# Performance work log

Measured on AMD Instinct MI355X. Metric: run time of the kernel, lower is better.

## Reference

```python
import jax, jax.numpy as jnp
import numpy as np

B, H, W = 4, 256, 256
DIM, DIM_OUT, NUM_HEADS = 96, 192, 3
WS = 8            # window_size
QS = 2            # q_stride (2,2)
HIDDEN = int(DIM_OUT * 4.0)
EPS = 1e-6


def layernorm(x, g, b):
    m = jnp.mean(x, axis=-1, keepdims=True)
    v = jnp.mean(jnp.square(x - m), axis=-1, keepdims=True)
    return (x - m) * jax.lax.rsqrt(v + EPS) * g + b


def maxpool2x2(x):
    # x: [..., h, w, c] -> [..., h//2, w//2, c]
    s = x.shape
    x = x.reshape(s[:-3] + (s[-3] // QS, QS, s[-2] // QS, QS, s[-1]))
    return x.max(axis=(-4, -2))


def setup_inputs() -> dict:
    key = jax.random.key(0)
    ks = jax.random.split(key, 16)
    std = 0.02
    return {
        "x": jax.random.normal(ks[0], (B, H, W, DIM), dtype=jnp.float32),
        "norm1_g": jnp.ones((DIM,), jnp.float32),
        "norm1_b": jnp.zeros((DIM,), jnp.float32),
        "proj_w": jax.random.normal(ks[1], (DIM, DIM_OUT), jnp.float32) * std,
        "proj_b": jnp.zeros((DIM_OUT,), jnp.float32),
        "qkv_w": jax.random.normal(ks[2], (DIM, 3 * DIM_OUT), jnp.float32) * std,
        "qkv_b": jnp.zeros((3 * DIM_OUT,), jnp.float32),
        "attn_proj_w": jax.random.normal(ks[3], (DIM_OUT, DIM_OUT), jnp.float32) * std,
        "attn_proj_b": jnp.zeros((DIM_OUT,), jnp.float32),
        "norm2_g": jnp.ones((DIM_OUT,), jnp.float32),
        "norm2_b": jnp.zeros((DIM_OUT,), jnp.float32),
        "mlp_w1": jax.random.normal(ks[4], (DIM_OUT, HIDDEN), jnp.float32) * std,
        "mlp_b1": jnp.zeros((HIDDEN,), jnp.float32),
        "mlp_w2": jax.random.normal(ks[5], (HIDDEN, DIM_OUT), jnp.float32) * std,
        "mlp_b2": jnpp_zeros if False else jnp.zeros((DIM_OUT,), jnp.float32),
    }


def reference(x, norm1_g, norm1_b, proj_w, proj_b, qkv_w, qkv_b,
              attn_proj_w, attn_proj_b, norm2_g, norm2_b,
              mlp_w1, mlp_b1, mlp_w2, mlp_b2):
    b, h, w, _ = x.shape
    xn = layernorm(x, norm1_g, norm1_b)

    # dim != dim_out: shortcut = proj(norm(x)), then pooled by q_stride
    shortcut = xn @ proj_w + proj_b                       # [B,H,W,Do]
    shortcut = maxpool2x2(shortcut)                       # [B,H/2,W/2,Do]

    # window partition (H,W divisible by WS -> no padding)
    nh, nw = h // WS, w // WS
    xw = xn.reshape(b, nh, WS, nw, WS, DIM).transpose(0, 1, 3, 2, 4, 5)
    xw = xw.reshape(b * nh * nw, WS, WS, DIM)             # [Bw,WS,WS,C]
    Bw = xw.shape[0]

    # MultiScaleAttention with q pooling
    hd = DIM_OUT // NUM_HEADS
    qkv = (xw @ qkv_w + qkv_b).reshape(Bw, WS * WS, 3, NUM_HEADS, hd)
    q, k, v = qkv[:, :, 0], qkv[:, :, 1], qkv[:, :, 2]    # [Bw,N,h,d]
    q = maxpool2x2(q.reshape(Bw, WS, WS, DIM_OUT))        # [Bw,WS/2,WS/2,Do]
    wq = WS // QS
    q = q.reshape(Bw, wq * wq, NUM_HEADS, hd)

    scale = 1.0 / jnp.sqrt(jnp.asarray(hd, x.dtype))
    scores = jnp.einsum('bqhd,bkhd->bhqk', q, k) * scale
    probs = jax.nn.softmax(scores, axis=-1)
    out = jnp.einsum('bhqk,bkhd->bqhd', probs, v).reshape(Bw, wq, wq, DIM_OUT)
    out = out @ attn_proj_w + attn_proj_b                 # [Bw,wq,wq,Do]

    # window unpartition at pooled resolution
    hp, wp = h // QS, w // QS
    out = out.reshape(b, nh, nw, wq, wq, DIM_OUT).transpose(0, 1, 3, 2, 4, 5)
    out = out.reshape(b, hp, wp, DIM_OUT)

    y = shortcut + out
    yn = layernorm(y, norm2_g, norm2_b)
    mlp = jax.nn.gelu(yn @ mlp_w1 + mlp_b1, approximate=False) @ mlp_w2 + mlp_b2
    return y + mlp
```

## Files before the change

kernel.cpp:

```cpp
#include <hip/hip_runtime.h>
#include <hip/hip_bf16.h>
#include <math.h>

#define EPSV 1e-6f

typedef __attribute__((ext_vector_type(8))) short bf16x8;
typedef __attribute__((ext_vector_type(4))) float f32x4;
typedef __attribute__((ext_vector_type(4))) unsigned short u16x4;
typedef __attribute__((ext_vector_type(2))) unsigned int u32x2;

__device__ inline float bf2f(unsigned short u) {
  union { unsigned int i; float f; } v;
  v.i = ((unsigned int)u) << 16;
  return v.f;
}
__device__ inline unsigned short f2bf(float f) {
  unsigned int u = __builtin_bit_cast(unsigned int, f);
  u += 0x7FFFu + ((u >> 16) & 1u);
  return (unsigned short)(u >> 16);
}
__device__ inline unsigned int pk2(float lo, float hi) {
  unsigned int r;
  asm("v_cvt_pk_bf16_f32 %0, %1, %2" : "=v"(r) : "v"(lo), "v"(hi));
  return r;
}
__device__ inline float fast_gelu(float v) {
  float u = 1.5957691216057308f * (v + 0.044715f * v * v * v);
  float t = __expf(-u);
  return v * __builtin_amdgcn_rcpf(1.f + t);
}

__global__ __launch_bounds__(256) void k0_pack(
    const float* __restrict__ qw, const float* __restrict__ aw,
    const float* __restrict__ w1, const float* __restrict__ w2,
    const float* __restrict__ pw, unsigned short* __restrict__ qwp,
    unsigned short* __restrict__ awp, unsigned short* __restrict__ w1p,
    unsigned short* __restrict__ w2p, unsigned short* __restrict__ pwp) {
  int idx = blockIdx.x * 256 + threadIdx.x;
  int lane = idx & 63;
  int l15 = lane & 15, quad = lane >> 4;
  if (idx < 6912) {
    int fi = idx >> 6;
    int ntile = fi / 3, kstep = fi - ntile * 3;
    int n = ntile * 16 + l15, k0 = kstep * 32 + quad * 8;
#pragma unroll
    for (int j = 0; j < 8; ++j)
      qwp[(size_t)idx * 8 + j] = f2bf(qw[(size_t)(k0 + j) * 576 + n]);
  } else if (idx < 11520) {
    int i2 = idx - 6912;
    int fi = i2 >> 6;
    int ntile = fi / 6, kstep = fi - ntile * 6;
    int n = ntile * 16 + l15, k0 = kstep * 32 + quad * 8;
#pragma unroll
    for (int j = 0; j < 8; ++j)
      awp[(size_t)i2 * 8 + j] = f2bf(aw[(size_t)(k0 + j) * 192 + n]);
  } else if (idx < 29952) {
    int i3 = idx - 11520;
    int fi = i3 >> 6;
    int ntile = fi / 6, kstep = fi - ntile * 6;
    int n = ntile * 16 + l15, k0 = kstep * 32 + quad * 8;
#pragma unroll
    for (int j = 0; j < 8; ++j)
      w1p[(size_t)i3 * 8 + j] = f2bf(w1[(size_t)(k0 + j) * 768 + n]);
  } else if (idx < 48384) {
    int i4 = idx - 29952;
    int fi = i4 >> 6;
    int ntile = fi / 24, kstep = fi - ntile * 24;
    int n = ntile * 16 + l15, k0 = kstep * 32 + quad * 8;
#pragma unroll
    for (int j = 0; j < 8; ++j)
      w2p[(size_t)i4 * 8 + j] = f2bf(w2[(size_t)(k0 + j) * 192 + n]);
  } else if (idx < 50688) {
    int i5 = idx - 48384;
    int fi = i5 >> 6;
    int ntile = fi / 3, kstep = fi - ntile * 3;
    int n = ntile * 16 + l15, k0 = kstep * 32 + quad * 8;
#pragma unroll
    for (int j = 0; j < 8; ++j)
      pwp[(size_t)i5 * 8 + j] = f2bf(pw[(size_t)(k0 + j) * 192 + n]);
  }
}

__global__ __launch_bounds__(256, 4) void k1234_fused(
    const float* __restrict__ x, const float* __restrict__ n1g,
    const float* __restrict__ n1b, const unsigned short* __restrict__ pwp,
    const float* __restrict__ pb, const unsigned short* __restrict__ qwp,
    const float* __restrict__ qb, const unsigned short* __restrict__ awp,
    const float* __restrict__ ab, const float* __restrict__ n2g,
    const float* __restrict__ n2b, const unsigned short* __restrict__ w1p,
    const float* __restrict__ b1, const unsigned short* __restrict__ w2p,
    const float* __restrict__ b2, float* __restrict__ out) {
  __shared__ __align__(16) unsigned char smem[39936];
  unsigned short (*kk)[200] = (unsigned short (*)[200])smem;
  unsigned short (*vT)[72] = (unsigned short (*)[72])smem;
  unsigned short (*yn)[200] = (unsigned short (*)[200])(smem + 6400);
  unsigned short (*hls)[200] = (unsigned short (*)[200])(smem + 12800);
  unsigned short (*wbuf)[16][72] =
      (unsigned short (*)[16][72])(smem + 27648);
  float (*sc)[192] = (float (*)[192])(smem + 27648);

  int tid = threadIdx.x, wave = tid >> 6, lane = tid & 63;
  int wi = blockIdx.x;
  int b = wi >> 10, nh = (wi >> 5) & 31, nw = wi & 31;
  int grow0 = nh * 8, gcol0 = nw * 8;
  int l15 = lane & 15, quad = lane >> 4;

  {
    int tt = tid >> 2, sub = tid & 3;
    int rr = tt >> 3, cc = tt & 7;
    size_t tok = (size_t)((b * 256 + grow0 + rr) * 256 + gcol0 + cc);
    const f32x4* xr4 = (const f32x4*)(x + tok * 96 + sub * 24);
    f32x4 v[6];
#pragma unroll
    for (int i = 0; i < 6; ++i) v[i] = xr4[i];
    float s = 0.f;
#pragma unroll
    for (int i = 0; i < 6; ++i)
#pragma unroll
      for (int j = 0; j < 4; ++j) s += v[i][j];
    s += __shfl_xor(s, 1);
    s += __shfl_xor(s, 2);
    float mean = s * (1.f / 96.f);
    float q = 0.f;
#pragma unroll
    for (int i = 0; i < 6; ++i)
#pragma unroll
      for (int j = 0; j < 4; ++j) {
        float d = v[i][j] - mean;
        q += d * d;
      }
    q += __shfl_xor(q, 1);
    q += __shfl_xor(q, 2);
    float rstd = rsqrtf(q * (1.f / 96.f) + EPSV);
    const f32x4* g4 = (const f32x4*)(n1g + sub * 24);
    const f32x4* b4 = (const f32x4*)(n1b + sub * 24);
#pragma unroll
    for (int i = 0; i < 6; ++i) {
      f32x4 gg = g4[i], bb = b4[i];
      u32x2 w;
      w[0] = pk2((v[i][0] - mean) * rstd * gg[0] + bb[0],
                 (v[i][1] - mean) * rstd * gg[1] + bb[1]);
      w[1] = pk2((v[i][2] - mean) * rstd * gg[2] + bb[2],
                 (v[i][3] - mean) * rstd * gg[3] + bb[3]);
      *(u32x2*)(&kk[tt][sub * 24 + i * 4]) = w;
    }
  }
  __syncthreads();

  bf16x8 areg[4][3];
#pragma unroll
  for (int mt = 0; mt < 4; ++mt)
#pragma unroll
    for (int ks = 0; ks < 3; ++ks)
      areg[mt][ks] = *(const bf16x8*)(&kk[mt * 16 + l15][ks * 32 + quad * 8]);
  __syncthreads();

#pragma unroll
  for (int aj = 0; aj < 6; ++aj) {
    int type, hh, nt;
    if (wave < 3) {
      if (aj < 4) { type = 0; hh = wave; nt = aj; }
      else { int kidx = wave * 2 + (aj - 4); type = 1; hh = kidx >> 2; nt = kidx & 3; }
    } else {
      int kidx = 6 + aj; type = 1; hh = kidx >> 2; nt = kidx & 3;
    }
    int gnt = type * 12 + hh * 4 + nt;
    const unsigned short* bp = qwp + (size_t)gnt * 1536 + lane * 8;
    bf16x8 b0 = *(const bf16x8*)(bp);
    bf16x8 b1v = *(const bf16x8*)(bp + 512);
    bf16x8 b2v = *(const bf16x8*)(bp + 1024);
    int dloc = nt * 16 + l15;
    int dglob = hh * 64 + dloc;
    float bias = qb[type * 192 + dglob];
#pragma unroll
    for (int mt = 0; mt < 4; ++mt) {
      f32x4 acc = {0.f, 0.f, 0.f, 0.f};
      acc = __builtin_amdgcn_mfma_f32_16x16x32_bf16(areg[mt][0], b0, acc, 0, 0, 0);
      acc = __builtin_amdgcn_mfma_f32_16x16x32_bf16(areg[mt][1], b1v, acc, 0, 0, 0);
      acc = __builtin_amdgcn_mfma_f32_16x16x32_bf16(areg[mt][2], b2v, acc, 0, 0, 0);
      if (type == 0) {
        float p0 = fmaxf(acc[0], acc[1]);
        float p1 = fmaxf(acc[2], acc[3]);
        float q0 = fmaxf(p0, __shfl_xor(p0, 32));
        float q1 = fmaxf(p1, __shfl_xor(p1, 32));
        unsigned int uq = pk2(q0 + bias, q1 + bias);
        if (quad < 2) {
          int p = mt * 4 + quad * 2;
          wbuf[wave][p][dloc] = (unsigned short)uq;
          wbuf[wave][p + 1][dloc] = (unsigned short)(uq >> 16);
        }
      } else {
        int t0 = mt * 16 + quad * 4;
        unsigned int u01 = pk2(acc[0] + bias, acc[1] + bias);
        unsigned int u23 = pk2(acc[2] + bias, acc[3] + bias);
        kk[t0 + 0][dglob] = (unsigned short)u01;
        kk[t0 + 1][dglob] = (unsigned short)(u01 >> 16);
        kk[t0 + 2][dglob] = (unsigned short)u23;
        kk[t0 + 3][dglob] = (unsigned short)(u23 >> 16);
      }
    }
  }
  __syncthreads();

  if (wave < 3) {
    int h = wave;
    bf16x8 aq0 = *(const bf16x8*)(&wbuf[wave][l15][quad * 8]);
    bf16x8 aq1 = *(const bf16x8*)(&wbuf[wave][l15][32 + quad * 8]);
    f32x4 s4[4];
#pragma unroll
    for (int kt = 0; kt < 4; ++kt) {
      bf16x8 bk0 = *(const bf16x8*)(&kk[kt * 16 + l15][h * 64 + quad * 8]);
      bf16x8 bk1 = *(const bf16x8*)(&kk[kt * 16 + l15][h * 64 + 32 + quad * 8]);
      f32x4 s = {0.f, 0.f, 0.f, 0.f};
      s = __builtin_amdgcn_mfma_f32_16x16x32_bf16(aq0, bk0, s, 0, 0, 0);
      s = __builtin_amdgcn_mfma_f32_16x16x32_bf16(aq1, bk1, s, 0, 0, 0);
      s4[kt] = s;
    }
    float ps[4][4];
#pragma unroll
    for (int r = 0; r < 4; ++r) {
      float m = fmaxf(fmaxf(s4[0][r], s4[1][r]), fmaxf(s4[2][r], s4[3][r]));
#pragma unroll
      for (int o = 8; o; o >>= 1) m = fmaxf(m, __shfl_xor(m, o));
      float sm = 0.f;
#pragma unroll
      for (int kt = 0; kt < 4; ++kt) {
        float e = __expf((s4[kt][r] - m) * 0.125f);
        ps[kt][r] = e;
        sm += e;
      }
#pragma unroll
      for (int o = 8; o; o >>= 1) sm += __shfl_xor(sm, o);
      float inv = __builtin_amdgcn_rcpf(sm);
#pragma unroll
      for (int kt = 0; kt < 4; ++kt) ps[kt][r] *= inv;
    }
#pragma unroll
    for (int r = 0; r < 4; ++r) {
      int row = quad * 4 + r;
      unsigned int u0 = pk2(ps[0][r], ps[1][r]);
      unsigned int u1 = pk2(ps[2][r], ps[3][r]);
      wbuf[wave][row][l15] = (unsigned short)u0;
      wbuf[wave][row][16 + l15] = (unsigned short)(u0 >> 16);
      wbuf[wave][row][32 + l15] = (unsigned short)u1;
      wbuf[wave][row][48 + l15] = (unsigned short)(u1 >> 16);
    }
  }
  __syncthreads();

#pragma unroll
  for (int vj = 0; vj < 3; ++vj) {
    int vidx = wave * 3 + vj;
    int hh = vidx >> 2, nt = vidx & 3;
    const unsigned short* bp =
        qwp + (size_t)(24 + hh * 4 + nt) * 1536 + lane * 8;
    bf16x8 b0 = *(const bf16x8*)(bp);
    bf16x8 b1v = *(const bf16x8*)(bp + 512);
    bf16x8 b2v = *(const bf16x8*)(bp + 1024);
    int dglob = hh * 64 + nt * 16 + l15;
    float bias = qb[384 + dglob];
#pragma unroll
    for (int mt = 0; mt < 4; ++mt) {
      f32x4 acc = {0.f, 0.f, 0.f, 0.f};
      acc = __builtin_amdgcn_mfma_f32_16x16x32_bf16(areg[mt][0], b0, acc, 0, 0, 0);
      acc = __builtin_amdgcn_mfma_f32_16x16x32_bf16(areg[mt][1], b1v, acc, 0, 0, 0);
      acc = __builtin_amdgcn_mfma_f32_16x16x32_bf16(areg[mt][2], b2v, acc, 0, 0, 0);
      int t0 = mt * 16 + quad * 4;
      u32x2 pk;
      pk[0] = pk2(acc[0] + bias, acc[1] + bias);
      pk[1] = pk2(acc[2] + bias, acc[3] + bias);
      *(u32x2*)(&vT[dglob][t0]) = pk;
    }
  }
  __syncthreads();

  f32x4 o4[4];
  if (wave < 3) {
    int h = wave;
    bf16x8 ap0 = *(const bf16x8*)(&wbuf[wave][l15][quad * 8]);
    bf16x8 ap1 = *(const bf16x8*)(&wbuf[wave][l15][32 + quad * 8]);
#pragma unroll
    for (int dt = 0; dt < 4; ++dt) {
      bf16x8 bv0 = *(const bf16x8*)(&vT[h * 64 + dt * 16 + l15][quad * 8]);
      bf16x8 bv1 = *(const bf16x8*)(&vT[h * 64 + dt * 16 + l15][32 + quad * 8]);
      f32x4 o = {0.f, 0.f, 0.f, 0.f};
      o = __builtin_amdgcn_mfma_f32_16x16x32_bf16(ap0, bv0, o, 0, 0, 0);
      o = __builtin_amdgcn_mfma_f32_16x16x32_bf16(ap1, bv1, o, 0, 0, 0);
      o4[dt] = o;
    }
  }
  __syncthreads();

  if (wave < 3) {
    int h = wave;
#pragma unroll
    for (int r = 0; r < 4; ++r) {
      int row = quad * 4 + r;
      unsigned int u0 = pk2(o4[0][r], o4[1][r]);
      unsigned int u1 = pk2(o4[2][r], o4[3][r]);
      kk[row][h * 64 + l15] = (unsigned short)u0;
      kk[row][h * 64 + 16 + l15] = (unsigned short)(u0 >> 16);
      kk[row][h * 64 + 32 + l15] = (unsigned short)u1;
      kk[row][h * 64 + 48 + l15] = (unsigned short)(u1 >> 16);
    }
  }
#pragma unroll
  for (int nl = 0; nl < 3; ++nl) {
    int nt = wave * 3 + nl;
    const unsigned short* bp = pwp + ((size_t)(nt * 3) * 64 + lane) * 8;
    bf16x8 b0 = *(const bf16x8*)(bp);
    bf16x8 b1v = *(const bf16x8*)(bp + 512);
    bf16x8 b2v = *(const bf16x8*)(bp + 1024);
    int c = nt * 16 + l15;
    float bias = pb[c];
#pragma unroll
    for (int mt = 0; mt < 4; ++mt) {
      f32x4 acc = {0.f, 0.f, 0.f, 0.f};
      acc = __builtin_amdgcn_mfma_f32_16x16x32_bf16(areg[mt][0], b0, acc, 0, 0, 0);
      acc = __builtin_amdgcn_mfma_f32_16x16x32_bf16(areg[mt][1], b1v, acc, 0, 0, 0);
      acc = __builtin_amdgcn_mfma_f32_16x16x32_bf16(areg[mt][2], b2v, acc, 0, 0, 0);
      float p0 = fmaxf(acc[0], acc[1]);
      float p1 = fmaxf(acc[2], acc[3]);
      float q0 = fmaxf(p0, __shfl_xor(p0, 32)) + bias;
      float q1 = fmaxf(p1, __shfl_xor(p1, 32)) + bias;
      if (quad < 2) {
        int p = mt * 4 + quad * 2;
        sc[p][c] = q0;
        sc[p + 1][c] = q1;
      }
    }
  }
  __syncthreads();

  bf16x8 ao[6];
#pragma unroll
  for (int ks = 0; ks < 6; ++ks)
    ao[ks] = *(const bf16x8*)(&kk[l15][ks * 32 + quad * 8]);
#pragma unroll
  for (int nl = 0; nl < 3; ++nl) {
    int ntl = wave * 3 + nl;
    const unsigned short* bp = awp + (size_t)ntl * 3072 + lane * 8;
    f32x4 acc = {0.f, 0.f, 0.f, 0.f};
#pragma unroll
    for (int ks = 0; ks < 6; ++ks) {
      bf16x8 bw = *(const bf16x8*)(bp + ks * 512);
      acc = __builtin_amdgcn_mfma_f32_16x16x32_bf16(ao[ks], bw, acc, 0, 0, 0);
    }
    int cc = ntl * 16 + l15;
    float bias = ab[cc];
#pragma unroll
    for (int r = 0; r < 4; ++r) {
      int p = quad * 4 + r;
      sc[p][cc] += acc[r] + bias;
    }
  }
  __syncthreads();

  {
    int tt = wave * 4 + quad;
    const f32x4* y4 = (const f32x4*)(&sc[tt][l15 * 12]);
    f32x4 vv[3];
    vv[0] = y4[0]; vv[1] = y4[1]; vv[2] = y4[2];
    float s = 0.f;
#pragma unroll
    for (int i = 0; i < 3; ++i)
#pragma unroll
      for (int j = 0; j < 4; ++j) s += vv[i][j];
    s += __shfl_xor(s, 1);
    s += __shfl_xor(s, 2);
    s += __shfl_xor(s, 4);
    s += __shfl_xor(s, 8);
    float mean = s * (1.f / 192.f);
    float q = 0.f;
#pragma unroll
    for (int i = 0; i < 3; ++i)
#pragma unroll
      for (int j = 0; j < 4; ++j) {
        float d = vv[i][j] - mean;
        q += d * d;
      }
    q += __shfl_xor(q, 1);
    q += __shfl_xor(q, 2);
    q += __shfl_xor(q, 4);
    q += __shfl_xor(q, 8);
    float rstd = rsqrtf(q * (1.f / 192.f) + EPSV);
    const f32x4* g4 = (const f32x4*)(n2g + l15 * 12);
    const f32x4* b4 = (const f32x4*)(n2b + l15 * 12);
#pragma unroll
    for (int i = 0; i < 3; ++i) {
      f32x4 gg = g4[i], bb = b4[i];
      u32x2 w;
      w[0] = pk2((vv[i][0] - mean) * rstd * gg[0] + bb[0],
                 (vv[i][1] - mean) * rstd * gg[1] + bb[1]);
      w[1] = pk2((vv[i][2] - mean) * rstd * gg[2] + bb[2],
                 (vv[i][3] - mean) * rstd * gg[3] + bb[3]);
      *(u32x2*)(&yn[tt][l15 * 12 + i * 4]) = w;
    }
  }
  __syncthreads();

  bf16x8 ar[6];
#pragma unroll
  for (int ks = 0; ks < 6; ++ks)
    ar[ks] = *(const bf16x8*)(&yn[l15][ks * 32 + quad * 8]);

  f32x4 acc2[3];
#pragma unroll
  for (int nl = 0; nl < 3; ++nl) acc2[nl] = (f32x4){0.f, 0.f, 0.f, 0.f};

  for (int c = 0; c < 4; ++c) {
#pragma unroll
    for (int nl = 0; nl < 3; ++nl) {
      int gnt = c * 12 + wave * 3 + nl;
      const unsigned short* bp = w1p + ((size_t)(gnt * 6) * 64 + lane) * 8;
      f32x4 t0 = {0.f, 0.f, 0.f, 0.f};
#pragma unroll
      for (int ks = 0; ks < 6; ++ks) {
        bf16x8 bw = *(const bf16x8*)(bp + ks * 512);
        t0 = __builtin_amdgcn_mfma_f32_16x16x32_bf16(ar[ks], bw, t0, 0, 0, 0);
      }
      int lcol = wave * 48 + nl * 16 + l15;
      float bias = b1[c * 192 + lcol];
      unsigned int u0 = pk2(fast_gelu(t0[0] + bias), fast_gelu(t0[1] + bias));
      unsigned int u1 = pk2(fast_gelu(t0[2] + bias), fast_gelu(t0[3] + bias));
      hls[quad * 4 + 0][lcol] = (unsigned short)u0;
      hls[quad * 4 + 1][lcol] = (unsigned short)(u0 >> 16);
      hls[quad * 4 + 2][lcol] = (unsigned short)u1;
      hls[quad * 4 + 3][lcol] = (unsigned short)(u1 >> 16);
    }
    __syncthreads();
    bf16x8 hr[6];
#pragma unroll
    for (int ks = 0; ks < 6; ++ks)
      hr[ks] = *(const bf16x8*)(&hls[l15][ks * 32 + quad * 8]);
#pragma unroll
    for (int nl = 0; nl < 3; ++nl) {
      int nt2 = wave * 3 + nl;
      const unsigned short* bp =
          w2p + ((size_t)(nt2 * 24 + c * 6) * 64 + lane) * 8;
#pragma unroll
      for (int ks = 0; ks < 6; ++ks) {
        bf16x8 bw = *(const bf16x8*)(bp + ks * 512);
        acc2[nl] =
            __builtin_amdgcn_mfma_f32_16x16x32_bf16(hr[ks], bw, acc2[nl], 0, 0, 0);
      }
    }
    __syncthreads();
  }

#pragma unroll
  for (int nl = 0; nl < 3; ++nl) {
    int col = (wave * 3 + nl) * 16 + l15;
    float bias = b2[col];
#pragma unroll
    for (int r = 0; r < 4; ++r) {
      int p = quad * 4 + r;
      int hp = nh * 4 + (p >> 2), wp2 = nw * 4 + (p & 3);
      size_t oi = ((size_t)((b * 128 + hp) * 128 + wp2)) * 192 + col;
      out[oi] = sc[p][col] + acc2[nl][r] + bias;
    }
  }
}

extern "C" void kernel_launch(void* const* d_in, const int* in_sizes, int n_in,
                              void* d_out, int out_size, void* d_ws,
                              size_t ws_size, hipStream_t stream) {
  const float* x = (const float*)d_in[0];
  const float* n1g = (const float*)d_in[1];
  const float* n1b = (const float*)d_in[2];
  const float* pw = (const float*)d_in[3];
  const float* pb = (const float*)d_in[4];
  const float* qw = (const float*)d_in[5];
  const float* qb = (const float*)d_in[6];
  const float* aw = (const float*)d_in[7];
  const float* ab = (const float*)d_in[8];
  const float* n2g = (const float*)d_in[9];
  const float* n2b = (const float*)d_in[10];
  const float* w1 = (const float*)d_in[11];
  const float* b1 = (const float*)d_in[12];
  const float* w2 = (const float*)d_in[13];
  const float* b2 = (const float*)d_in[14];
  float* out = (float*)d_out;

  char* wsb = (char*)d_ws;
  unsigned short* qwp = (unsigned short*)wsb;
  unsigned short* awp = (unsigned short*)(wsb + 110592);
  unsigned short* w1p = (unsigned short*)(wsb + 184320);
  unsigned short* w2p = (unsigned short*)(wsb + 479232);
  unsigned short* pwp = (unsigned short*)(wsb + 774144);

  hipLaunchKernelGGL(k0_pack, dim3(198), dim3(256), 0, stream, qw, aw, w1, w2,
                     pw, qwp, awp, w1p, w2p, pwp);
  hipLaunchKernelGGL(k1234_fused, dim3(4096), dim3(256), 0, stream, x, n1g,
                     n1b, pwp, pb, qwp, qb, awp, ab, n2g, n2b, w1p, b1, w2p,
                     b2, out);
}
```

Measured before the change: 309.9 us.

## Fuse shortcut projection into QKV loop and halve MLP hidden chunk count

```diff
diff --git a/kernel.cpp b/kernel.cpp
--- a/kernel.cpp
+++ b/kernel.cpp
@@ -90,14 +90,14 @@
     const float* __restrict__ n2b, const unsigned short* __restrict__ w1p,
     const float* __restrict__ b1, const unsigned short* __restrict__ w2p,
     const float* __restrict__ b2, float* __restrict__ out) {
-  __shared__ __align__(16) unsigned char smem[39936];
+  __shared__ __align__(16) unsigned char smem[40192];
   unsigned short (*kk)[200] = (unsigned short (*)[200])smem;
   unsigned short (*vT)[72] = (unsigned short (*)[72])smem;
   unsigned short (*yn)[200] = (unsigned short (*)[200])(smem + 6400);
-  unsigned short (*hls)[200] = (unsigned short (*)[200])(smem + 12800);
+  unsigned short (*hls)[392] = (unsigned short (*)[392])(smem + 12800);
   unsigned short (*wbuf)[16][72] =
       (unsigned short (*)[16][72])(smem + 27648);
-  float (*sc)[192] = (float (*)[192])(smem + 27648);
+  float (*sc)[196] = (float (*)[196])(smem + 27648);
 
   int tid = threadIdx.x, wave = tid >> 6, lane = tid & 63;
   int wi = blockIdx.x;
@@ -155,23 +155,32 @@
       areg[mt][ks] = *(const bf16x8*)(&kk[mt * 16 + l15][ks * 32 + quad * 8]);
   __syncthreads();
 
-#pragma unroll
-  for (int aj = 0; aj < 6; ++aj) {
+  float scr[3][4][2];
+#pragma unroll
+  for (int aj = 0; aj < 9; ++aj) {
     int type, hh, nt;
-    if (wave < 3) {
+    if (aj >= 6) {
+      type = 2; hh = 0; nt = aj - 6;
+    } else if (wave < 3) {
       if (aj < 4) { type = 0; hh = wave; nt = aj; }
       else { int kidx = wave * 2 + (aj - 4); type = 1; hh = kidx >> 2; nt = kidx & 3; }
     } else {
       int kidx = 6 + aj; type = 1; hh = kidx >> 2; nt = kidx & 3;
     }
-    int gnt = type * 12 + hh * 4 + nt;
-    const unsigned short* bp = qwp + (size_t)gnt * 1536 + lane * 8;
+    const unsigned short* bp;
+    float bias;
+    if (type == 2) {
+      int pnt = wave * 3 + nt;
+      bp = pwp + ((size_t)(pnt * 3) * 64 + lane) * 8;
+      bias = pb[pnt * 16 + l15];
+    } else {
+      int gnt = type * 12 + hh * 4 + nt;
+      bp = qwp + (size_t)gnt * 1536 + lane * 8;
+      bias = qb[type * 192 + hh * 64 + nt * 16 + l15];
+    }
     bf16x8 b0 = *(const bf16x8*)(bp);
     bf16x8 b1v = *(const bf16x8*)(bp + 512);
     bf16x8 b2v = *(const bf16x8*)(bp + 1024);
-    int dloc = nt * 16 + l15;
-    int dglob = hh * 64 + dloc;
-    float bias = qb[type * 192 + dglob];
 #pragma unroll
     for (int mt = 0; mt < 4; ++mt) {
       f32x4 acc = {0.f, 0.f, 0.f, 0.f};
@@ -186,10 +195,11 @@
         unsigned int uq = pk2(q0 + bias, q1 + bias);
         if (quad < 2) {
           int p = mt * 4 + quad * 2;
-          wbuf[wave][p][dloc] = (unsigned short)uq;
-          wbuf[wave][p + 1][dloc] = (unsigned short)(uq >> 16);
+          wbuf[wave][p][nt * 16 + l15] = (unsigned short)uq;
+          wbuf[wave][p + 1][nt * 16 + l15] = (unsigned short)(uq >> 16);
         }
-      } else {
+      } else if (type == 1) {
+        int dglob = hh * 64 + nt * 16 + l15;
         int t0 = mt * 16 + quad * 4;
         unsigned int u01 = pk2(acc[0] + bias, acc[1] + bias);
         unsigned int u23 = pk2(acc[2] + bias, acc[3] + bias);
@@ -197,6 +207,11 @@
         kk[t0 + 1][dglob] = (unsigned short)(u01 >> 16);
         kk[t0 + 2][dglob] = (unsigned short)u23;
         kk[t0 + 3][dglob] = (unsigned short)(u23 >> 16);
+      } else {
+        float p0 = fmaxf(acc[0], acc[1]);
+        float p1 = fmaxf(acc[2], acc[3]);
+        scr[nt][mt][0] = fmaxf(p0, __shfl_xor(p0, 32)) + bias;
+        scr[nt][mt][1] = fmaxf(p1, __shfl_xor(p1, 32)) + bias;
       }
     }
   }
@@ -216,30 +231,23 @@
       s = __builtin_amdgcn_mfma_f32_16x16x32_bf16(aq1, bk1, s, 0, 0, 0);
       s4[kt] = s;
     }
-    float ps[4][4];
 #pragma unroll
     for (int r = 0; r < 4; ++r) {
+      float ps0, ps1, ps2, ps3;
       float m = fmaxf(fmaxf(s4[0][r], s4[1][r]), fmaxf(s4[2][r], s4[3][r]));
 #pragma unroll
       for (int o = 8; o; o >>= 1) m = fmaxf(m, __shfl_xor(m, o));
-      float sm = 0.f;
-#pragma unroll
-      for (int kt = 0; kt < 4; ++kt) {
-        float e = __expf((s4[kt][r] - m) * 0.125f);
-        ps[kt][r] = e;
-        sm += e;
-      }
+      ps0 = __expf((s4[0][r] - m) * 0.125f);
+      ps1 = __expf((s4[1][r] - m) * 0.125f);
+      ps2 = __expf((s4[2][r] - m) * 0.125f);
+      ps3 = __expf((s4[3][r] - m) * 0.125f);
+      float sm = ps0 + ps1 + ps2 + ps3;
 #pragma unroll
       for (int o = 8; o; o >>= 1) sm += __shfl_xor(sm, o);
       float inv = __builtin_amdgcn_rcpf(sm);
-#pragma unroll
-      for (int kt = 0; kt < 4; ++kt) ps[kt][r] *= inv;
-    }
-#pragma unroll
-    for (int r = 0; r < 4; ++r) {
       int row = quad * 4 + r;
-      unsigned int u0 = pk2(ps[0][r], ps[1][r]);
-      unsigned int u1 = pk2(ps[2][r], ps[3][r]);
+      unsigned int u0 = pk2(ps0 * inv, ps1 * inv);
+      unsigned int u1 = pk2(ps2 * inv, ps3 * inv);
       wbuf[wave][row][l15] = (unsigned short)u0;
       wbuf[wave][row][16 + l15] = (unsigned short)(u0 >> 16);
       wbuf[wave][row][32 + l15] = (unsigned short)u1;
@@ -304,29 +312,15 @@
       kk[row][h * 64 + 48 + l15] = (unsigned short)(u1 >> 16);
     }
   }
-#pragma unroll
-  for (int nl = 0; nl < 3; ++nl) {
-    int nt = wave * 3 + nl;
-    const unsigned short* bp = pwp + ((size_t)(nt * 3) * 64 + lane) * 8;
-    bf16x8 b0 = *(const bf16x8*)(bp);
-    bf16x8 b1v = *(const bf16x8*)(bp + 512);
-    bf16x8 b2v = *(const bf16x8*)(bp + 1024);
-    int c = nt * 16 + l15;
-    float bias = pb[c];
-#pragma unroll
-    for (int mt = 0; mt < 4; ++mt) {
-      f32x4 acc = {0.f, 0.f, 0.f, 0.f};
-      acc = __builtin_amdgcn_mfma_f32_16x16x32_bf16(areg[mt][0], b0, acc, 0, 0, 0);
-      acc = __builtin_amdgcn_mfma_f32_16x16x32_bf16(areg[mt][1], b1v, acc, 0, 0, 0);
-      acc = __builtin_amdgcn_mfma_f32_16x16x32_bf16(areg[mt][2], b2v, acc, 0, 0, 0);
-      float p0 = fmaxf(acc[0], acc[1]);
-      float p1 = fmaxf(acc[2], acc[3]);
-      float q0 = fmaxf(p0, __shfl_xor(p0, 32)) + bias;
-      float q1 = fmaxf(p1, __shfl_xor(p1, 32)) + bias;
-      if (quad < 2) {
+  if (quad < 2) {
+#pragma unroll
+    for (int nl = 0; nl < 3; ++nl) {
+      int c = (wave * 3 + nl) * 16 + l15;
+#pragma unroll
+      for (int mt = 0; mt < 4; ++mt) {
         int p = mt * 4 + quad * 2;
-        sc[p][c] = q0;
-        sc[p + 1][c] = q1;
+        sc[p][c] = scr[nl][mt][0];
+        sc[p + 1][c] = scr[nl][mt][1];
       }
     }
   }
@@ -408,10 +402,11 @@
 #pragma unroll
   for (int nl = 0; nl < 3; ++nl) acc2[nl] = (f32x4){0.f, 0.f, 0.f, 0.f};
 
-  for (int c = 0; c < 4; ++c) {
-#pragma unroll
-    for (int nl = 0; nl < 3; ++nl) {
-      int gnt = c * 12 + wave * 3 + nl;
+#pragma unroll
+  for (int c = 0; c < 2; ++c) {
+#pragma unroll
+    for (int nl = 0; nl < 6; ++nl) {
+      int gnt = c * 24 + wave * 6 + nl;
       const unsigned short* bp = w1p + ((size_t)(gnt * 6) * 64 + lane) * 8;
       f32x4 t0 = {0.f, 0.f, 0.f, 0.f};
 #pragma unroll
@@ -419,8 +414,8 @@
         bf16x8 bw = *(const bf16x8*)(bp + ks * 512);
         t0 = __builtin_amdgcn_mfma_f32_16x16x32_bf16(ar[ks], bw, t0, 0, 0, 0);
       }
-      int lcol = wave * 48 + nl * 16 + l15;
-      float bias = b1[c * 192 + lcol];
+      int lcol = wave * 96 + nl * 16 + l15;
+      float bias = b1[c * 384 + lcol];
       unsigned int u0 = pk2(fast_gelu(t0[0] + bias), fast_gelu(t0[1] + bias));
       unsigned int u1 = pk2(fast_gelu(t0[2] + bias), fast_gelu(t0[3] + bias));
       hls[quad * 4 + 0][lcol] = (unsigned short)u0;
@@ -429,23 +424,26 @@
       hls[quad * 4 + 3][lcol] = (unsigned short)(u1 >> 16);
     }
     __syncthreads();
-    bf16x8 hr[6];
-#pragma unroll
-    for (int ks = 0; ks < 6; ++ks)
-      hr[ks] = *(const bf16x8*)(&hls[l15][ks * 32 + quad * 8]);
-#pragma unroll
-    for (int nl = 0; nl < 3; ++nl) {
-      int nt2 = wave * 3 + nl;
-      const unsigned short* bp =
-          w2p + ((size_t)(nt2 * 24 + c * 6) * 64 + lane) * 8;
-#pragma unroll
-      for (int ks = 0; ks < 6; ++ks) {
-        bf16x8 bw = *(const bf16x8*)(bp + ks * 512);
-        acc2[nl] =
-            __builtin_amdgcn_mfma_f32_16x16x32_bf16(hr[ks], bw, acc2[nl], 0, 0, 0);
-      }
-    }
-    __syncthreads();
+#pragma unroll
+    for (int g = 0; g < 2; ++g) {
+      bf16x8 hr[6];
+#pragma unroll
+      for (int ks = 0; ks < 6; ++ks)
+        hr[ks] = *(const bf16x8*)(&hls[l15][(g * 6 + ks) * 32 + quad * 8]);
+#pragma unroll
+      for (int nl = 0; nl < 3; ++nl) {
+        int nt2 = wave * 3 + nl;
+        const unsigned short* bp =
+            w2p + ((size_t)(nt2 * 24 + c * 12 + g * 6) * 64 + lane) * 8;
+#pragma unroll
+        for (int ks = 0; ks < 6; ++ks) {
+          bf16x8 bw = *(const bf16x8*)(bp + ks * 512);
+          acc2[nl] =
+              __builtin_amdgcn_mfma_f32_16x16x32_bf16(hr[ks], bw, acc2[nl], 0, 0, 0);
+        }
+      }
+    }
+    if (c == 0) __syncthreads();
   }
 
 #pragma unroll
```

Result: slower. 411.0 us (+32.6%).
